# Performance work log

Measured on AMD Instinct MI355X. Metric: run time of the kernel, lower is better.

Reference implementation:

```python
import jax, jax.numpy as jnp
import numpy as np

NUM_HEADS = 8

def setup_inputs() -> dict:
    key = jax.random.key(0)
    k0, k1, k2, k3 = jax.random.split(key, 4)
    B, C, H, W = 2, 512, 64, 64
    x = jax.random.normal(k0, (B, C, H, W), dtype=jnp.float32)
    # binary ROI mask (hard mode): 1 inside region, 0 outside
    mask = (jax.random.uniform(k1, (B, 1, H, W)) > 0.5).astype(jnp.float32)
    Wqkv = jax.random.normal(k2, (3 * C, C), dtype=jnp.float32) * 0.02
    bqkv = jnp.zeros((3 * C,), dtype=jnp.float32)
    Wproj = jax.random.normal(k3, (C, C), dtype=jnp.float32) * 0.02
    bproj = jnp.zeros((C,), dtype=jnp.float32)
    return {"x": x, "mask": mask, "Wqkv": Wqkv, "bqkv": bqkv, "Wproj": Wproj, "bproj": bproj}


def reference(x, mask, Wqkv, bqkv, Wproj, bproj):
    B, C, H, W = x.shape
    N = H * W
    d = C // NUM_HEADS
    scale = d ** (-0.5)

    xf = x.reshape(B, C, N)
    # 1x1 conv == per-pixel linear: [3C,C] @ [B,C,N]
    qkv = jnp.einsum('oc,bcn->bon', Wqkv, xf) + bqkv[None, :, None]
    q, k, v = jnp.split(qkv, 3, axis=1)  # each [B,C,N]

    def to_heads(t):  # [B,C,N] -> [B,h,N,d]
        return t.reshape(B, NUM_HEADS, d, N).transpose(0, 1, 3, 2)

    q, k, v = to_heads(q), to_heads(k), to_heads(v)

    attn = jnp.einsum('bhnd,bhmd->bhnm', q, k) * scale  # [B,h,N,N]
    # hard mask bias: -10000 on keys outside ROI, broadcast over query dim
    roi = mask.reshape(B, 1, 1, N)
    attn = attn + (1.0 - roi) * (-10000.0)
    attn = jax.nn.softmax(attn, axis=-1)
    # attn_drop = 0.0 -> identity

    out = jnp.einsum('bhnm,bhmd->bhnd', attn, v)  # [B,h,N,d]
    out = out.transpose(0, 1, 3, 2).reshape(B, C, N)
    out = jnp.einsum('oc,bcn->bon', Wproj, out) + bproj[None, :, None]
    return out.reshape(B, C, H, W)
```

## Files before the change

kernel.cpp:

```cpp
#include <hip/hip_runtime.h>

#define BB 2
#define CC 512
#define NH 8
#define DDIM 64
#define NN 4096
#define QSCALE 0.18033688011112042f
#define MBIAS  -14426.950408889634f

typedef __bf16 bfx8 __attribute__((ext_vector_type(8)));
typedef __bf16 bf2  __attribute__((ext_vector_type(2)));
typedef float  f32x4 __attribute__((ext_vector_type(4)));
typedef int    i32x4 __attribute__((ext_vector_type(4)));

__device__ inline ushort f2bf(float f) {
  return __builtin_bit_cast(ushort, (__bf16)f);
}

__device__ __forceinline__ void gload_lds16(const void* g, void* l) {
  __builtin_amdgcn_global_load_lds(
      (const __attribute__((address_space(1))) void*)g,
      (__attribute__((address_space(3))) void*)l, 16, 0, 0);
}

__device__ __forceinline__ void swap32(int& a, int& b) {
  asm("v_permlane32_swap_b32 %0, %1" : "+v"(a), "+v"(b));
}
__device__ __forceinline__ void swap16(int& a, int& b) {
  asm("v_permlane16_swap_b32 %0, %1" : "+v"(a), "+v"(b));
}

__global__ __launch_bounds__(256)
void convert_w(const float* __restrict__ Wqkv, const float* __restrict__ Wproj,
               ushort* __restrict__ Wq, ushort* __restrict__ Wp) {
    const int n1 = (1536*CC)/4;
    const int n2 = (CC*CC)/4;
    int i = blockIdx.x*256 + threadIdx.x;
    if (i < n1) {
        float4 v = *(const float4*)(&Wqkv[(size_t)i*4]);
        if (i < 65536) { v.x*=QSCALE; v.y*=QSCALE; v.z*=QSCALE; v.w*=QSCALE; }
        ushort4 o; o.x=f2bf(v.x); o.y=f2bf(v.y); o.z=f2bf(v.z); o.w=f2bf(v.w);
        *(ushort4*)(&Wq[(size_t)i*4]) = o;
    } else if (i < n1+n2) {
        int j = i - n1;
        float4 v = *(const float4*)(&Wproj[(size_t)j*4]);
        ushort4 o; o.x=f2bf(v.x); o.y=f2bf(v.y); o.z=f2bf(v.z); o.w=f2bf(v.w);
        *(ushort4*)(&Wp[(size_t)j*4]) = o;
    }
}

__global__ __launch_bounds__(256)
void transpose_x(const float* __restrict__ x, ushort* __restrict__ xT) {
    const int bn = blockIdx.x, bc = blockIdx.y, b = blockIdx.z;
    const int t = threadIdx.x;
    __shared__ float T[64][65];
    const int n0 = bn*64, c0 = bc*64;
    const int tc = t >> 4, tn4 = (t & 15) * 4;
    #pragma unroll
    for (int r = 0; r < 4; ++r) {
        int c = tc + r*16;
        float4 v = *(const float4*)(&x[((size_t)b*CC + c0 + c)*NN + n0 + tn4]);
        T[c][tn4+0] = v.x; T[c][tn4+1] = v.y; T[c][tn4+2] = v.z; T[c][tn4+3] = v.w;
    }
    __syncthreads();
    #pragma unroll
    for (int r = 0; r < 4; ++r) {
        int n = tc + r*16;
        ushort4 o;
        o.x = f2bf(T[tn4+0][n]); o.y = f2bf(T[tn4+1][n]);
        o.z = f2bf(T[tn4+2][n]); o.w = f2bf(T[tn4+3][n]);
        *(ushort4*)(&xT[((size_t)b*NN + n0 + n)*CC + c0 + tn4]) = o;
    }
}

__global__ __launch_bounds__(256)
void qkv_mfma(const ushort* __restrict__ xT, const ushort* __restrict__ Wb,
              const float* __restrict__ bias, ushort* __restrict__ qws,
              ushort* __restrict__ kws, ushort* __restrict__ vws) {
    const int bn = blockIdx.x;
    const int bo = blockIdx.y;
    const int b  = blockIdx.z;
    const int t  = threadIdx.x;
    const int w  = t >> 6, l = t & 63, g = l >> 4, m = l & 15;
    const int o0 = bo * 128, n0 = bn * 128;
    const int part = o0 >> 9;
    const int wr = w >> 1, wc = w & 1;

    __shared__ __align__(16) ushort Xs[128*64];
    __shared__ __align__(16) ushort Ws_[128*64];

    const ushort* xbase = xT + ((size_t)b*NN + n0)*CC;
    const ushort* wbase = Wb + (size_t)o0*CC;

    f32x4 acc[4][4];
    #pragma unroll
    for (int i=0;i<4;i++)
        #pragma unroll
        for (int j=0;j<4;j++) acc[i][j] = (f32x4){0.f,0.f,0.f,0.f};

    const ushort* R = (part < 2) ? Xs  : Ws_;
    const ushort* Cc = (part < 2) ? Ws_ : Xs;

    for (int k0 = 0; k0 < CC; k0 += 64) {
        #pragma unroll
        for (int it = 0; it < 4; ++it) {
            int c16 = (it*4 + w)*64 + l;
            int row = c16 >> 3;
            int gch = (c16 & 7) ^ (row & 7);
            gload_lds16(xbase + (size_t)row*CC + k0 + gch*8, Xs  + c16*8);
            gload_lds16(wbase + (size_t)row*CC + k0 + gch*8, Ws_ + c16*8);
        }
        __syncthreads();
        __builtin_amdgcn_s_setprio(1);
        #pragma unroll
        for (int kc = 0; kc < 2; ++kc) {
            bfx8 ra[4], cb[4];
            #pragma unroll
            for (int f = 0; f < 4; ++f) {
                int rrow = wr*64 + f*16 + m;
                ra[f] = *(const bfx8*)(R  + (rrow*8 + ((kc*4+g) ^ (rrow&7)))*8);
                int crow = wc*64 + f*16 + m;
                cb[f] = *(const bfx8*)(Cc + (crow*8 + ((kc*4+g) ^ (crow&7)))*8);
            }
            #pragma unroll
            for (int i = 0; i < 4; ++i)
                #pragma unroll
                for (int j = 0; j < 4; ++j)
                    acc[i][j] = __builtin_amdgcn_mfma_f32_16x16x32_bf16(ra[i], cb[j], acc[i][j], 0, 0, 0);
        }
        __builtin_amdgcn_s_setprio(0);
        __syncthreads();
    }

    if (part < 2) {
        ushort* dst = (part == 0) ? qws : kws;
        const float bs = (part == 0) ? QSCALE : 1.f;
        #pragma unroll
        for (int j = 0; j < 4; ++j) {
            int o = o0 + wc*64 + j*16 + m;
            int ol = o & 511;
            int h = ol >> 6, d = ol & 63;
            float bv = bias[o] * bs;
            ushort* dp = dst + ((size_t)b*NH + h)*(size_t)NN*DDIM + d;
            #pragma unroll
            for (int i = 0; i < 4; ++i)
                #pragma unroll
                for (int r = 0; r < 4; ++r) {
                    int n = n0 + wr*64 + i*16 + g*4 + r;
                    dp[(size_t)n*DDIM] = f2bf(acc[i][j][r] + bv);
                }
        }
    } else {
        #pragma unroll
        for (int i = 0; i < 4; ++i)
            #pragma unroll
            for (int r = 0; r < 4; ++r) {
                int o = o0 + wr*64 + i*16 + g*4 + r;
                int vo = o - 1024;
                int h = vo >> 6, d = vo & 63;
                float bv = bias[o];
                ushort* dp = vws + (((size_t)b*NH + h)*DDIM + d)*NN;
                #pragma unroll
                for (int j = 0; j < 4; ++j) {
                    int n = n0 + wc*64 + j*16 + m;
                    dp[n] = f2bf(acc[i][j][r] + bv);
                }
            }
    }
}

__global__ __launch_bounds__(256, 4)
void attn_mfma(const ushort* __restrict__ qw, const ushort* __restrict__ kw,
               const ushort* __restrict__ vw, const float* __restrict__ mask,
               ushort* __restrict__ aob) {
    const int qt = blockIdx.x, h = blockIdx.y, b = blockIdx.z;
    const int t = threadIdx.x;
    const int w = t >> 6, l = t & 63, g = l >> 4, m = l & 15;
    const int n0 = qt * 64;
    const size_t bh = (size_t)b * NH + h;
    const ushort* qp = qw + bh * (size_t)NN * DDIM;
    const ushort* kp = kw + bh * (size_t)NN * DDIM;
    const ushort* vp = vw + bh * (size_t)DDIM * NN;

    __shared__ __align__(16) ushort Ks[2][64*64];
    __shared__ __align__(16) ushort Vs[2][64*64];
    __shared__ float mb[2][64];

    bfx8 qf[2];
    #pragma unroll
    for (int kc = 0; kc < 2; ++kc)
        qf[kc] = *(const bfx8*)(qp + (size_t)(n0 + w*16 + m)*DDIM + kc*32 + g*8);

    f32x4 o[4];
    #pragma unroll
    for (int f=0; f<4; ++f) o[f] = (f32x4){0.f,0.f,0.f,0.f};
    float m_run = -1e30f;
    float l_part = 0.f;

    float4 kreg0, kreg1, vreg0, vreg1;
    float mreg = 0.f;
    kreg0 = *(const float4*)(kp + (size_t)t*8);
    kreg1 = *(const float4*)(kp + (size_t)(t+256)*8);
    vreg0 = *(const float4*)(vp + (size_t)(t>>3)*NN + (t&7)*8);
    vreg1 = *(const float4*)(vp + (size_t)((t+256)>>3)*NN + ((t+256)&7)*8);
    if (t < 64) mreg = mask[(size_t)b*NN + t];
    {
        int row = t >> 3, c = t & 7;
        *(float4*)(&Ks[0][row*64 + ((c ^ (row&7))*8)]) = kreg0;
        *(float4*)(&Vs[0][row*64 + ((c ^ (row&7))*8)]) = vreg0;
        int t1 = t + 256, row1 = t1 >> 3, c1 = t1 & 7;
        *(float4*)(&Ks[0][row1*64 + ((c1 ^ (row1&7))*8)]) = kreg1;
        *(float4*)(&Vs[0][row1*64 + ((c1 ^ (row1&7))*8)]) = vreg1;
        if (t < 64) mb[0][t] = (1.f - mreg) * MBIAS;
    }
    {
        const int nb = 64;
        kreg0 = *(const float4*)(kp + (size_t)nb*DDIM + t*8);
        kreg1 = *(const float4*)(kp + (size_t)nb*DDIM + (t+256)*8);
        vreg0 = *(const float4*)(vp + (size_t)(t>>3)*NN + nb + (t&7)*8);
        vreg1 = *(const float4*)(vp + (size_t)((t+256)>>3)*NN + nb + ((t+256)&7)*8);
        if (t < 64) mreg = mask[(size_t)b*NN + nb + t];
    }

    for (int kt = 0; kt < 64; ++kt) {
        const int cur = kt & 1, nxt = cur ^ 1;
        __syncthreads();
        if (kt + 1 < 64) {
            int row = t >> 3, c = t & 7;
            *(float4*)(&Ks[nxt][row*64 + ((c ^ (row&7))*8)]) = kreg0;
            *(float4*)(&Vs[nxt][row*64 + ((c ^ (row&7))*8)]) = vreg0;
            int t1 = t + 256, row1 = t1 >> 3, c1 = t1 & 7;
            *(float4*)(&Ks[nxt][row1*64 + ((c1 ^ (row1&7))*8)]) = kreg1;
            *(float4*)(&Vs[nxt][row1*64 + ((c1 ^ (row1&7))*8)]) = vreg1;
            if (t < 64) mb[nxt][t] = (1.f - mreg) * MBIAS;
        }
        if (kt + 2 < 64) {
            const int nb = (kt + 2) * 64;
            kreg0 = *(const float4*)(kp + (size_t)nb*DDIM + t*8);
            kreg1 = *(const float4*)(kp + (size_t)nb*DDIM + (t+256)*8);
            vreg0 = *(const float4*)(vp + (size_t)(t>>3)*NN + nb + (t&7)*8);
            vreg1 = *(const float4*)(vp + (size_t)((t+256)>>3)*NN + nb + ((t+256)&7)*8);
            if (t < 64) mreg = mask[(size_t)b*NN + nb + t];
        }

        f32x4 sa[4];
        #pragma unroll
        for (int f=0; f<4; ++f) sa[f] = (f32x4){0.f,0.f,0.f,0.f};
        __builtin_amdgcn_s_setprio(1);
        #pragma unroll
        for (int kc=0; kc<2; ++kc)
            #pragma unroll
            for (int f=0; f<4; ++f) {
                int row = f*16 + m;
                bfx8 kf = *(const bfx8*)(&Ks[cur][row*64 + ((kc*32 + g*8) ^ ((row&7)*8))]);
                sa[f] = __builtin_amdgcn_mfma_f32_16x16x32_bf16(kf, qf[kc], sa[f], 0, 0, 0);
            }
        __builtin_amdgcn_s_setprio(0);

        float sv[4][4];
        #pragma unroll
        for (int f=0; f<4; ++f) {
            float4 mbv = *(const float4*)(&mb[cur][f*16 + 4*g]);
            sv[f][0] = sa[f][0] + mbv.x;
            sv[f][1] = sa[f][1] + mbv.y;
            sv[f][2] = sa[f][2] + mbv.z;
            sv[f][3] = sa[f][3] + mbv.w;
        }
        float tmax = sv[0][0];
        #pragma unroll
        for (int f=0; f<4; ++f)
            #pragma unroll
            for (int r=0; r<4; ++r) tmax = fmaxf(tmax, sv[f][r]);
        tmax = fmaxf(tmax, __shfl_xor(tmax, 16));
        tmax = fmaxf(tmax, __shfl_xor(tmax, 32));

        if (__any(tmax > m_run + 8.f)) {
            float mnew = fmaxf(m_run, tmax);
            float alpha = __builtin_amdgcn_exp2f(m_run - mnew);
            m_run = mnew;
            l_part *= alpha;
            float ar[4];
            #pragma unroll
            for (int r=0; r<4; ++r) ar[r] = __shfl(alpha, 4*g + r);
            #pragma unroll
            for (int f=0; f<4; ++f)
                #pragma unroll
                for (int r=0; r<4; ++r) o[f][r] *= ar[r];
        }

        float pv_[4][4];
        float tsum = 0.f;
        #pragma unroll
        for (int f=0; f<4; ++f)
            #pragma unroll
            for (int r=0; r<4; ++r) {
                float p = __builtin_amdgcn_exp2f(sv[f][r] - m_run);
                pv_[f][r] = p;
                tsum += p;
            }
        l_part += tsum;

        int u[4][2];
        #pragma unroll
        for (int f=0; f<4; ++f)
            #pragma unroll
            for (int pp=0; pp<2; ++pp) {
                bf2 tpk = { (__bf16)pv_[f][2*pp], (__bf16)pv_[f][2*pp+1] };
                u[f][pp] = __builtin_bit_cast(int, tpk);
            }
        #pragma unroll
        for (int pp=0; pp<2; ++pp) { swap32(u[0][pp], u[1][pp]); swap32(u[2][pp], u[3][pp]); }
        #pragma unroll
        for (int pp=0; pp<2; ++pp) { swap16(u[0][pp], u[1][pp]); swap16(u[2][pp], u[3][pp]); }
        bfx8 pa[2];
        pa[0] = __builtin_bit_cast(bfx8, (i32x4){u[0][0], u[0][1], u[1][0], u[1][1]});
        pa[1] = __builtin_bit_cast(bfx8, (i32x4){u[2][0], u[2][1], u[3][0], u[3][1]});

        __builtin_amdgcn_s_setprio(1);
        #pragma unroll
        for (int kc=0; kc<2; ++kc)
            #pragma unroll
            for (int f=0; f<4; ++f) {
                int row = f*16 + m;
                bfx8 vf = *(const bfx8*)(&Vs[cur][row*64 + ((kc*32 + g*8) ^ ((row&7)*8))]);
                o[f] = __builtin_amdgcn_mfma_f32_16x16x32_bf16(pa[kc], vf, o[f], 0, 0, 0);
            }
        __builtin_amdgcn_s_setprio(0);
    }

    float l_tot = l_part + __shfl_xor(l_part, 16);
    l_tot += __shfl_xor(l_tot, 32);
    float linv = 1.f / l_tot;
    float lr[4];
    #pragma unroll
    for (int r=0; r<4; ++r) lr[r] = __shfl(linv, 4*g + r);
    #pragma unroll
    for (int f=0; f<4; ++f)
        #pragma unroll
        for (int r=0; r<4; ++r)
            aob[((size_t)b*NN + n0 + w*16 + 4*g + r)*CC + h*DDIM + f*16 + m] = f2bf(o[f][r] * lr[r]);
}

__global__ __launch_bounds__(256)
void proj_mfma(const ushort* __restrict__ aob, const ushort* __restrict__ Wp,
               const float* __restrict__ bias, float* __restrict__ out) {
    const int bn = blockIdx.x;
    const int bo = blockIdx.y;
    const int b  = blockIdx.z;
    const int t  = threadIdx.x;
    const int w  = t >> 6, l = t & 63, g = l >> 4, m = l & 15;
    const int o0 = bo * 128, n0 = bn * 128;
    const int wr = w >> 1, wc = w & 1;

    __shared__ __align__(16) ushort As_[128*64];
    __shared__ __align__(16) ushort Ws_[128*64];

    const ushort* abase = aob + ((size_t)b*NN + n0)*CC;
    const ushort* wbase = Wp + (size_t)o0*CC;

    f32x4 acc[4][4];
    #pragma unroll
    for (int i=0;i<4;i++)
        #pragma unroll
        for (int j=0;j<4;j++) acc[i][j] = (f32x4){0.f,0.f,0.f,0.f};

    for (int k0 = 0; k0 < CC; k0 += 64) {
        #pragma unroll
        for (int it = 0; it < 4; ++it) {
            int c16 = (it*4 + w)*64 + l;
            int row = c16 >> 3;
            int gch = (c16 & 7) ^ (row & 7);
            gload_lds16(abase + (size_t)row*CC + k0 + gch*8, As_ + c16*8);
            gload_lds16(wbase + (size_t)row*CC + k0 + gch*8, Ws_ + c16*8);
        }
        __syncthreads();
        __builtin_amdgcn_s_setprio(1);
        #pragma unroll
        for (int kc = 0; kc < 2; ++kc) {
            bfx8 ra[4], cb[4];
            #pragma unroll
            for (int f = 0; f < 4; ++f) {
                int rrow = wr*64 + f*16 + m;
                ra[f] = *(const bfx8*)(Ws_ + (rrow*8 + ((kc*4+g) ^ (rrow&7)))*8);
                int crow = wc*64 + f*16 + m;
                cb[f] = *(const bfx8*)(As_ + (crow*8 + ((kc*4+g) ^ (crow&7)))*8);
            }
            #pragma unroll
            for (int i = 0; i < 4; ++i)
                #pragma unroll
                for (int j = 0; j < 4; ++j)
                    acc[i][j] = __builtin_amdgcn_mfma_f32_16x16x32_bf16(ra[i], cb[j], acc[i][j], 0, 0, 0);
        }
        __builtin_amdgcn_s_setprio(0);
        __syncthreads();
    }
    #pragma unroll
    for (int i = 0; i < 4; ++i)
        #pragma unroll
        for (int r = 0; r < 4; ++r) {
            int o = o0 + wr*64 + i*16 + g*4 + r;
            float bv = bias[o];
            float* dp = out + ((size_t)b*CC + o)*NN;
            #pragma unroll
            for (int j = 0; j < 4; ++j) {
                int n = n0 + wc*64 + j*16 + m;
                dp[n] = acc[i][j][r] + bv;
            }
        }
}

extern "C" void kernel_launch(void* const* d_in, const int* in_sizes, int n_in,
                              void* d_out, int out_size, void* d_ws, size_t ws_size,
                              hipStream_t stream) {
    const float* x     = (const float*)d_in[0];
    const float* mask  = (const float*)d_in[1];
    const float* Wqkv  = (const float*)d_in[2];
    const float* bqkv  = (const float*)d_in[3];
    const float* Wproj = (const float*)d_in[4];
    const float* bproj = (const float*)d_in[5];
    float* out = (float*)d_out;

    const size_t per = (size_t)BB*NH*NN*DDIM;
    ushort* qws = (ushort*)d_ws;
    ushort* kws = qws + per;
    ushort* vws = kws + per;
    ushort* xTb = vws + per;
    ushort* aob = xTb + per;
    ushort* Wqb = aob + per;
    ushort* Wpb = Wqb + (size_t)1536*CC;

    convert_w<<<dim3(1024), 256, 0, stream>>>(Wqkv, Wproj, Wqb, Wpb);
    transpose_x<<<dim3(64, 8, BB), 256, 0, stream>>>(x, xTb);
    qkv_mfma<<<dim3(32, 12, BB), 256, 0, stream>>>(xTb, Wqb, bqkv, qws, kws, vws);
    attn_mfma<<<dim3(64, NH, BB), 256, 0, stream>>>(qws, kws, vws, mask, aob);
    proj_mfma<<<dim3(32, 4, BB), 256, 0, stream>>>(aob, Wpb, bproj, out);
}
```

Baseline: 224.3 us.

## Double query rows per attention block and reorder QK store loop

```diff
diff --git a/kernel.cpp b/kernel.cpp
--- a/kernel.cpp
+++ b/kernel.cpp
@@ -135,21 +135,21 @@
     if (part < 2) {
         ushort* dst = (part == 0) ? qws : kws;
         const float bs = (part == 0) ? QSCALE : 1.f;
-        #pragma unroll
-        for (int j = 0; j < 4; ++j) {
-            int o = o0 + wc*64 + j*16 + m;
-            int ol = o & 511;
-            int h = ol >> 6, d = ol & 63;
-            float bv = bias[o] * bs;
-            ushort* dp = dst + ((size_t)b*NH + h)*(size_t)NN*DDIM + d;
-            #pragma unroll
-            for (int i = 0; i < 4; ++i)
-                #pragma unroll
-                for (int r = 0; r < 4; ++r) {
-                    int n = n0 + wr*64 + i*16 + g*4 + r;
-                    dp[(size_t)n*DDIM] = f2bf(acc[i][j][r] + bv);
-                }
-        }
+        const int h = ((o0 & 511) >> 6) + wc;
+        float bvj[4];
+        #pragma unroll
+        for (int j = 0; j < 4; ++j) bvj[j] = bias[o0 + wc*64 + j*16 + m] * bs;
+        ushort* base = dst + ((size_t)b*NH + h)*(size_t)NN*DDIM;
+        #pragma unroll
+        for (int i = 0; i < 4; ++i)
+            #pragma unroll
+            for (int r = 0; r < 4; ++r) {
+                int n = n0 + wr*64 + i*16 + g*4 + r;
+                ushort* rowp = base + (size_t)n*DDIM;
+                #pragma unroll
+                for (int j = 0; j < 4; ++j)
+                    rowp[j*16 + m] = f2bf(acc[i][j][r] + bvj[j]);
+            }
     } else {
         #pragma unroll
         for (int i = 0; i < 4; ++i)
@@ -169,14 +169,14 @@
     }
 }
 
-__global__ __launch_bounds__(256, 4)
+__global__ __launch_bounds__(256, 2)
 void attn_mfma(const ushort* __restrict__ qw, const ushort* __restrict__ kw,
                const ushort* __restrict__ vw, const float* __restrict__ mask,
                ushort* __restrict__ aob) {
     const int qt = blockIdx.x, h = blockIdx.y, b = blockIdx.z;
     const int t = threadIdx.x;
     const int w = t >> 6, l = t & 63, g = l >> 4, m = l & 15;
-    const int n0 = qt * 64;
+    const int n0 = qt * 128;
     const size_t bh = (size_t)b * NH + h;
     const ushort* qp = qw + bh * (size_t)NN * DDIM;
     const ushort* kp = kw + bh * (size_t)NN * DDIM;
@@ -186,16 +186,20 @@
     __shared__ __align__(16) ushort Vs[2][64*64];
     __shared__ float mb[2][64];
 
-    bfx8 qf[2];
-    #pragma unroll
-    for (int kc = 0; kc < 2; ++kc)
-        qf[kc] = *(const bfx8*)(qp + (size_t)(n0 + w*16 + m)*DDIM + kc*32 + g*8);
-
-    f32x4 o[4];
-    #pragma unroll
-    for (int f=0; f<4; ++f) o[f] = (f32x4){0.f,0.f,0.f,0.f};
-    float m_run = -1e30f;
-    float l_part = 0.f;
+    bfx8 qf[2][2];
+    #pragma unroll
+    for (int qi = 0; qi < 2; ++qi)
+        #pragma unroll
+        for (int kc = 0; kc < 2; ++kc)
+            qf[qi][kc] = *(const bfx8*)(qp + (size_t)(n0 + w*32 + qi*16 + m)*DDIM + kc*32 + g*8);
+
+    f32x4 o[2][4];
+    #pragma unroll
+    for (int qi=0; qi<2; ++qi)
+        #pragma unroll
+        for (int f=0; f<4; ++f) o[qi][f] = (f32x4){0.f,0.f,0.f,0.f};
+    float m_run[2] = {-1e30f, -1e30f};
+    float l_part[2] = {0.f, 0.f};
 
     float4 kreg0, kreg1, vreg0, vreg1;
     float mreg = 0.f;
@@ -243,9 +247,11 @@
             if (t < 64) mreg = mask[(size_t)b*NN + nb + t];
         }
 
-        f32x4 sa[4];
-        #pragma unroll
-        for (int f=0; f<4; ++f) sa[f] = (f32x4){0.f,0.f,0.f,0.f};
+        f32x4 sa[2][4];
+        #pragma unroll
+        for (int qi=0; qi<2; ++qi)
+            #pragma unroll
+            for (int f=0; f<4; ++f) sa[qi][f] = (f32x4){0.f,0.f,0.f,0.f};
         __builtin_amdgcn_s_setprio(1);
         #pragma unroll
         for (int kc=0; kc<2; ++kc)
@@ -253,68 +259,76 @@
             for (int f=0; f<4; ++f) {
                 int row = f*16 + m;
                 bfx8 kf = *(const bfx8*)(&Ks[cur][row*64 + ((kc*32 + g*8) ^ ((row&7)*8))]);
-                sa[f] = __builtin_amdgcn_mfma_f32_16x16x32_bf16(kf, qf[kc], sa[f], 0, 0, 0);
+                #pragma unroll
+                for (int qi=0; qi<2; ++qi)
+                    sa[qi][f] = __builtin_amdgcn_mfma_f32_16x16x32_bf16(kf, qf[qi][kc], sa[qi][f], 0, 0, 0);
             }
         __builtin_amdgcn_s_setprio(0);
 
-        float sv[4][4];
-        #pragma unroll
-        for (int f=0; f<4; ++f) {
-            float4 mbv = *(const float4*)(&mb[cur][f*16 + 4*g]);
-            sv[f][0] = sa[f][0] + mbv.x;
-            sv[f][1] = sa[f][1] + mbv.y;
-            sv[f][2] = sa[f][2] + mbv.z;
-            sv[f][3] = sa[f][3] + mbv.w;
-        }
-        float tmax = sv[0][0];
-        #pragma unroll
-        for (int f=0; f<4; ++f)
-            #pragma unroll
-            for (int r=0; r<4; ++r) tmax = fmaxf(tmax, sv[f][r]);
-        tmax = fmaxf(tmax, __shfl_xor(tmax, 16));
-        tmax = fmaxf(tmax, __shfl_xor(tmax, 32));
-
-        if (__any(tmax > m_run + 8.f)) {
-            float mnew = fmaxf(m_run, tmax);
-            float alpha = __builtin_amdgcn_exp2f(m_run - mnew);
-            m_run = mnew;
-            l_part *= alpha;
-            float ar[4];
-            #pragma unroll
-            for (int r=0; r<4; ++r) ar[r] = __shfl(alpha, 4*g + r);
+        float4 mbv[4];
+        #pragma unroll
+        for (int f=0; f<4; ++f) mbv[f] = *(const float4*)(&mb[cur][f*16 + 4*g]);
+
+        bfx8 pa[2][2];
+        #pragma unroll
+        for (int qi=0; qi<2; ++qi) {
+            float sv[4][4];
+            #pragma unroll
+            for (int f=0; f<4; ++f) {
+                sv[f][0] = sa[qi][f][0] + mbv[f].x;
+                sv[f][1] = sa[qi][f][1] + mbv[f].y;
+                sv[f][2] = sa[qi][f][2] + mbv[f].z;
+                sv[f][3] = sa[qi][f][3] + mbv[f].w;
+            }
+            float tmax = sv[0][0];
             #pragma unroll
             for (int f=0; f<4; ++f)
                 #pragma unroll
-                for (int r=0; r<4; ++r) o[f][r] *= ar[r];
-        }
-
-        float pv_[4][4];
-        float tsum = 0.f;
-        #pragma unroll
-        for (int f=0; f<4; ++f)
-            #pragma unroll
-            for (int r=0; r<4; ++r) {
-                float p = __builtin_amdgcn_exp2f(sv[f][r] - m_run);
-                pv_[f][r] = p;
-                tsum += p;
-            }
-        l_part += tsum;
-
-        int u[4][2];
-        #pragma unroll
-        for (int f=0; f<4; ++f)
-            #pragma unroll
-            for (int pp=0; pp<2; ++pp) {
-                bf2 tpk = { (__bf16)pv_[f][2*pp], (__bf16)pv_[f][2*pp+1] };
-                u[f][pp] = __builtin_bit_cast(int, tpk);
-            }
-        #pragma unroll
-        for (int pp=0; pp<2; ++pp) { swap32(u[0][pp], u[1][pp]); swap32(u[2][pp], u[3][pp]); }
-        #pragma unroll
-        for (int pp=0; pp<2; ++pp) { swap16(u[0][pp], u[1][pp]); swap16(u[2][pp], u[3][pp]); }
-        bfx8 pa[2];
-        pa[0] = __builtin_bit_cast(bfx8, (i32x4){u[0][0], u[0][1], u[1][0], u[1][1]});
-        pa[1] = __builtin_bit_cast(bfx8, (i32x4){u[2][0], u[2][1], u[3][0], u[3][1]});
+                for (int r=0; r<4; ++r) tmax = fmaxf(tmax, sv[f][r]);
+            tmax = fmaxf(tmax, __shfl_xor(tmax, 16));
+            tmax = fmaxf(tmax, __shfl_xor(tmax, 32));
+
+            if (__any(tmax > m_run[qi] + 8.f)) {
+                float mnew = fmaxf(m_run[qi], tmax);
+                float alpha = __builtin_amdgcn_exp2f(m_run[qi] - mnew);
+                m_run[qi] = mnew;
+                l_part[qi] *= alpha;
+                float ar[4];
+                #pragma unroll
+                for (int r=0; r<4; ++r) ar[r] = __shfl(alpha, 4*g + r);
+                #pragma unroll
+                for (int f=0; f<4; ++f)
+                    #pragma unroll
+                    for (int r=0; r<4; ++r) o[qi][f][r] *= ar[r];
+            }
+
+            float pv_[4][4];
+            float tsum = 0.f;
+            #pragma unroll
+            for (int f=0; f<4; ++f)
+                #pragma unroll
+                for (int r=0; r<4; ++r) {
+                    float p = __builtin_amdgcn_exp2f(sv[f][r] - m_run[qi]);
+                    pv_[f][r] = p;
+                    tsum += p;
+                }
+            l_part[qi] += tsum;
+
+            int u[4][2];
+            #pragma unroll
+            for (int f=0; f<4; ++f)
+                #pragma unroll
+                for (int pp=0; pp<2; ++pp) {
+                    bf2 tpk = { (__bf16)pv_[f][2*pp], (__bf16)pv_[f][2*pp+1] };
+                    u[f][pp] = __builtin_bit_cast(int, tpk);
+                }
+            #pragma unroll
+            for (int pp=0; pp<2; ++pp) { swap32(u[0][pp], u[1][pp]); swap32(u[2][pp], u[3][pp]); }
+            #pragma unroll
+            for (int pp=0; pp<2; ++pp) { swap16(u[0][pp], u[1][pp]); swap16(u[2][pp], u[3][pp]); }
+            pa[qi][0] = __builtin_bit_cast(bfx8, (i32x4){u[0][0], u[0][1], u[1][0], u[1][1]});
+            pa[qi][1] = __builtin_bit_cast(bfx8, (i32x4){u[2][0], u[2][1], u[3][0], u[3][1]});
+        }
 
         __builtin_amdgcn_s_setprio(1);
         #pragma unroll
@@ -323,22 +337,27 @@
             for (int f=0; f<4; ++f) {
                 int row = f*16 + m;
                 bfx8 vf = *(const bfx8*)(&Vs[cur][row*64 + ((kc*32 + g*8) ^ ((row&7)*8))]);
-                o[f] = __builtin_amdgcn_mfma_f32_16x16x32_bf16(pa[kc], vf, o[f], 0, 0, 0);
+                #pragma unroll
+                for (int qi=0; qi<2; ++qi)
+                    o[qi][f] = __builtin_amdgcn_mfma_f32_16x16x32_bf16(pa[qi][kc], vf, o[qi][f], 0, 0, 0);
             }
         __builtin_amdgcn_s_setprio(0);
     }
 
-    float l_tot = l_part + __shfl_xor(l_part, 16);
-    l_tot += __shfl_xor(l_tot, 32);
-    float linv = 1.f / l_tot;
-    float lr[4];
-    #pragma unroll
-    for (int r=0; r<4; ++r) lr[r] = __shfl(linv, 4*g + r);
-    #pragma unroll
-    for (int f=0; f<4; ++f)
-        #pragma unroll
-        for (int r=0; r<4; ++r)
-            aob[((size_t)b*NN + n0 + w*16 + 4*g + r)*CC + h*DDIM + f*16 + m] = f2bf(o[f][r] * lr[r]);
+    #pragma unroll
+    for (int qi=0; qi<2; ++qi) {
+        float l_tot = l_part[qi] + __shfl_xor(l_part[qi], 16);
+        l_tot += __shfl_xor(l_tot, 32);
+        float linv = 1.f / l_tot;
+        float lr[4];
+        #pragma unroll
+        for (int r=0; r<4; ++r) lr[r] = __shfl(linv, 4*g + r);
+        #pragma unroll
+        for (int f=0; f<4; ++f)
+            #pragma unroll
+            for (int r=0; r<4; ++r)
+                aob[((size_t)b*NN + n0 + w*32 + qi*16 + 4*g + r)*CC + h*DDIM + f*16 + m] = f2bf(o[qi][f][r] * lr[r]);
+    }
 }
 
 __global__ __launch_bounds__(256)
@@ -432,6 +451,6 @@
     convert_w<<<dim3(1024), 256, 0, stream>>>(Wqkv, Wproj, Wqb, Wpb);
     transpose_x<<<dim3(64, 8, BB), 256, 0, stream>>>(x, xTb);
     qkv_mfma<<<dim3(32, 12, BB), 256, 0, stream>>>(xTb, Wqb, bqkv, qws, kws, vws);
-    attn_mfma<<<dim3(64, NH, BB), 256, 0, stream>>>(qws, kws, vws, mask, aob);
+    attn_mfma<<<dim3(32, NH, BB), 256, 0, stream>>>(qws, kws, vws, mask, aob);
     proj_mfma<<<dim3(32, 4, BB), 256, 0, stream>>>(aob, Wpb, bproj, out);
 }
```

Result: faster. 215.0 us (-4.1%).
